# Performance work log

Measured on AMD Instinct MI355X. Metric: run time of the kernel, lower is better.

## Reference

```python
import jax, jax.numpy as jnp
import numpy as np

B, S, D = 1, 2048, 2048
H, KV, HD = 16, 4, 128
E, TOPK, F = 8, 2, 2048
THETA = 500000.0
CLIP = 8.0
EPS = 1e-5


def setup_inputs() -> dict:
    key = jax.random.key(0)
    ks = jax.random.split(key, 8)
    sc = 0.02
    return {
        "hidden_states": jax.random.normal(ks[0], (B, S, D), jnp.float32),
        "position_ids": jnp.arange(S, dtype=jnp.int64)[None, :].repeat(B, axis=0),
        "ln1_w": jnp.ones((D,), jnp.float32),
        "ln2_w": jnp.ones((D,), jnp.float32),
        "wqkv": jax.random.normal(ks[1], (D, (H + 2 * KV) * HD), jnp.float32) * sc,
        "wo": jax.random.normal(ks[2], (H * HD, D), jnp.float32) * sc,
        "router_w": jax.random.normal(ks[3], (E, D), jnp.float32) * sc,
        "w1": jax.random.normal(ks[4], (E, D, F), jnp.float32) * sc,
        "v1": jax.random.normal(ks[5], (E, D, F), jnp.float32) * sc,
        "w2": jax.random.normal(ks[6], (E, F, D), jnp.float32) * sc,
    }


def _layernorm(x, w):
    mu = jnp.mean(x, axis=-1, keepdims=True)
    var = jnp.mean((x - mu) ** 2, axis=-1, keepdims=True)
    return (x - mu) * jax.lax.rsqrt(var + EPS) * w


def _rotate_half(x):
    x1, x2 = jnp.split(x, 2, axis=-1)
    return jnp.concatenate([-x2, x1], axis=-1)


def _rope(pos):
    inv_freq = 1.0 / (THETA ** (jnp.arange(0, HD, 2, dtype=jnp.float32) / HD))
    ang = pos.astype(jnp.float32)[..., None] * inv_freq  # [B,S,HD/2]
    ang = jnp.concatenate([ang, ang], axis=-1)  # [B,S,HD]
    return jnp.cos(ang)[:, None], jnp.sin(ang)[:, None]  # [B,1,S,HD]


def _forward(hidden_states, position_ids, ln1_w, ln2_w, wqkv, wo, router_w, w1, v1, w2):
    x = hidden_states
    # --- attention sublayer ---
    h = _layernorm(x, ln1_w)
    qkv = jnp.clip(h @ wqkv, -CLIP, CLIP)  # [B,S,(H+2KV)*HD]
    q, k, v = jnp.split(qkv, [H * HD, (H + KV) * HD], axis=-1)
    q = q.reshape(B, S, H, HD).transpose(0, 2, 1, 3)   # [B,H,S,HD]
    k = k.reshape(B, S, KV, HD).transpose(0, 2, 1, 3)  # [B,KV,S,HD]
    v = v.reshape(B, S, KV, HD).transpose(0, 2, 1, 3)
    cos, sin = _rope(position_ids)
    q = q * cos + _rotate_half(q) * sin
    k = k * cos + _rotate_half(k) * sin
    rep = H // KV
    k = jnp.repeat(k, rep, axis=1)  # [B,H,S,HD]
    v = jnp.repeat(v, rep, axis=1)
    scores = jnp.einsum("bhqd,bhkd->bhqk", q, k) / np.sqrt(HD).astype(np.float32)
    causal = jnp.tril(jnp.ones((S, S), bool))
    scores = jnp.where(causal, scores, jnp.finfo(scores.dtype).min)
    probs = jax.nn.softmax(scores, axis=-1)
    attn = jnp.einsum("bhqk,bhkd->bhqd", probs, v)
    attn = attn.transpose(0, 2, 1, 3).reshape(B, S, H * HD) @ wo
    x = x + attn
    # --- MoE FFN sublayer ---
    h = _layernorm(x, ln2_w).reshape(B * S, D)  # [T,D]
    logits = h @ router_w.T                      # [T,E]
    rp = jax.nn.softmax(logits, axis=-1)
    top_w, top_i = jax.lax.top_k(rp, TOPK)       # [T,K]
    top_w = top_w / jnp.sum(top_w, axis=-1, keepdims=True)
    T = B * S
    gate = jnp.zeros((T, E), h.dtype).at[jnp.arange(T)[:, None], top_i].add(top_w)
    g = jax.nn.silu(jnp.einsum("td,edf->tef", h, w1)) * jnp.einsum("td,edf->tef", h, v1)
    y = jnp.einsum("tef,efd,te->td", g, w2, gate)
    x = x + y.reshape(B, S, D)
    return x


def reference(hidden_states, position_ids, ln1_w, ln2_w, wqkv, wo, router_w, w1, v1, w2):
    return _forward(hidden_states, position_ids, ln1_w, ln2_w, wqkv, wo, router_w, w1, v1, w2)
```

## Files before the change

### kernel.cpp

```cpp
#include <hip/hip_runtime.h>

#define S_LEN 2048
#define DMODEL 2048
#define NH 16
#define NKV 4
#define HD 128
#define NE 8
#define FF 2048
#define QKV_N 3072

typedef __attribute__((ext_vector_type(8))) short short8;
typedef __attribute__((ext_vector_type(4))) float f32x4;

__device__ inline unsigned short f2bf(float f) {
  unsigned int u = __builtin_bit_cast(unsigned int, f);
  u += 0x7fffu + ((u >> 16) & 1u);
  return (unsigned short)(u >> 16);
}
__device__ inline float bf2f(unsigned short h) {
  unsigned int u = ((unsigned int)h) << 16;
  return __builtin_bit_cast(float, u);
}
__device__ inline void split2(float v, unsigned short& h, unsigned short& l) {
  h = f2bf(v);
  l = f2bf(v - bf2f(h));
}


__device__ inline void gload16(const void* g, void* l) {
  __builtin_amdgcn_global_load_lds((const __attribute__((address_space(1))) unsigned int*)g,
                                   (__attribute__((address_space(3))) unsigned int*)l,
                                   16, 0, 0);
}
__device__ inline void stageB_chunk(const unsigned short* __restrict__ chunk,
                                    unsigned short* __restrict__ lds) {
  int w = threadIdx.x >> 6, l = threadIdx.x & 63;
  const unsigned short* s = chunk + w * 1024 + l * 8;
  unsigned short* d = lds + w * 1024;
  gload16(s, d);
  gload16(s + 512, d + 512);
}

#define WAIT_ALL  asm volatile("s_waitcnt vmcnt(0) lgkmcnt(0)" ::: "memory")
#define WAIT_LDS  asm volatile("s_waitcnt lgkmcnt(0)" ::: "memory")
#define SCHEDBAR  __builtin_amdgcn_sched_barrier(0)
#define BAR       __builtin_amdgcn_s_barrier()


__device__ inline void mma16(const unsigned short* As, const unsigned short* Bs,
                             int wr, int wc, f32x4 acc[4][4]) {
  int l = threadIdx.x & 63;
  int lr = l & 15, lg = l >> 4;
  int qoff = ((lg ^ ((lr ^ (lr >> 2)) & 3)) << 3);
  short8 a[4], b[4];
#pragma unroll
  for (int m = 0; m < 4; m++)
    a[m] = *(const short8*)(As + (wr + m * 16 + lr) * 32 + qoff);
#pragma unroll
  for (int n = 0; n < 4; n++)
    b[n] = *(const short8*)(Bs + (wc + n * 16 + lr) * 32 + qoff);
#pragma unroll
  for (int m = 0; m < 4; m++)
#pragma unroll
    for (int n = 0; n < 4; n++)
      acc[m][n] = __builtin_amdgcn_mfma_f32_16x16x32_bf16(a[m], b[n], acc[m][n], 0, 0, 0);
}

__device__ inline void mma16_dualB(const unsigned short* As, const unsigned short* Bs1,
                                   const unsigned short* Bs2, int wr, int wc,
                                   f32x4 acc1[4][4], f32x4 acc2[4][4]) {
  int l = threadIdx.x & 63;
  int lr = l & 15, lg = l >> 4;
  int qoff = ((lg ^ ((lr ^ (lr >> 2)) & 3)) << 3);
  short8 a[4], b1[4], b2[4];
#pragma unroll
  for (int m = 0; m < 4; m++)
    a[m] = *(const short8*)(As + (wr + m * 16 + lr) * 32 + qoff);
#pragma unroll
  for (int n = 0; n < 4; n++) {
    b1[n] = *(const short8*)(Bs1 + (wc + n * 16 + lr) * 32 + qoff);
    b2[n] = *(const short8*)(Bs2 + (wc + n * 16 + lr) * 32 + qoff);
  }
#pragma unroll
  for (int m = 0; m < 4; m++)
#pragma unroll
    for (int n = 0; n < 4; n++) {
      acc1[m][n] = __builtin_amdgcn_mfma_f32_16x16x32_bf16(a[m], b1[n], acc1[m][n], 0, 0, 0);
      acc2[m][n] = __builtin_amdgcn_mfma_f32_16x16x32_bf16(a[m], b2[n], acc2[m][n], 0, 0, 0);
    }
}

__device__ inline void mma16_split_reg(const unsigned short* Ash, const unsigned short* Asl,
                                       const unsigned short* Bsh, const unsigned short* Bsl,
                                       int wr, int wc, f32x4 acc[4][4]) {
  int l = threadIdx.x & 63;
  int lr = l & 15, lg = l >> 4;
  int qoff = ((lg ^ ((lr ^ (lr >> 2)) & 3)) << 3);
  short8 ah[4], al[4], bh[4], bl[4];
#pragma unroll
  for (int m = 0; m < 4; m++) {
    ah[m] = *(const short8*)(Ash + (wr + m * 16 + lr) * 32 + qoff);
    al[m] = *(const short8*)(Asl + (wr + m * 16 + lr) * 32 + qoff);
  }
#pragma unroll
  for (int n = 0; n < 4; n++) {
    bh[n] = *(const short8*)(Bsh + (wc + n * 16 + lr) * 32 + qoff);
    bl[n] = *(const short8*)(Bsl + (wc + n * 16 + lr) * 32 + qoff);
  }
#pragma unroll
  for (int m = 0; m < 4; m++)
#pragma unroll
    for (int n = 0; n < 4; n++) {
      acc[m][n] = __builtin_amdgcn_mfma_f32_16x16x32_bf16(ah[m], bh[n], acc[m][n], 0, 0, 0);
      acc[m][n] = __builtin_amdgcn_mfma_f32_16x16x32_bf16(ah[m], bl[n], acc[m][n], 0, 0, 0);
      acc[m][n] = __builtin_amdgcn_mfma_f32_16x16x32_bf16(al[m], bh[n], acc[m][n], 0, 0, 0);
    }
}


__global__ __launch_bounds__(256) void k_pack1(const float* __restrict__ src, long ld,
                                               long zs, int nc,
                                               unsigned short* __restrict__ dst) {
  __shared__ float tile[32][132];
  const float* Sp = src + (long)blockIdx.z * zs;
  int c = blockIdx.x, t = threadIdx.x;
  for (int i = 0; i < 4; i++) {
    int kt = blockIdx.y * 4 + i;
    long k0 = (long)kt * 32, n0 = (long)c * 128;
    {
      int k = t >> 3, nn = (t & 7) * 16;
      const float4* p = (const float4*)(Sp + (k0 + k) * ld + n0 + nn);
#pragma unroll
      for (int j = 0; j < 4; j++) *(float4*)&tile[k][nn + j * 4] = p[j];
    }
    __syncthreads();
    size_t cbase = ((size_t)(blockIdx.z * nc + c) * 64 + kt) * 4096;
#pragma unroll
    for (int uu = 0; uu < 2; uu++) {
      int u = t * 2 + uu;
      int n = u >> 2, qp = u & 3;
      int q = qp ^ ((n ^ (n >> 2)) & 3);
      unsigned short hb[8] __attribute__((aligned(16)));
#pragma unroll
      for (int j = 0; j < 8; j++) hb[j] = f2bf(tile[8 * q + j][n]);
      *(uint4*)(dst + cbase + u * 8) = *(const uint4*)hb;
    }
    __syncthreads();
  }
}

__global__ __launch_bounds__(256) void k_pack2(const float* __restrict__ src, long ld,
                                               long zs, int nc,
                                               unsigned short* __restrict__ dh,
                                               unsigned short* __restrict__ dl) {
  __shared__ float tile[32][132];
  const float* Sp = src + (long)blockIdx.z * zs;
  int c = blockIdx.x, t = threadIdx.x;
  for (int i = 0; i < 4; i++) {
    int kt = blockIdx.y * 4 + i;
    long k0 = (long)kt * 32, n0 = (long)c * 128;
    {
      int k = t >> 3, nn = (t & 7) * 16;
      const float4* p = (const float4*)(Sp + (k0 + k) * ld + n0 + nn);
#pragma unroll
      for (int j = 0; j < 4; j++) *(float4*)&tile[k][nn + j * 4] = p[j];
    }
    __syncthreads();
    size_t cbase = ((size_t)(blockIdx.z * nc + c) * 64 + kt) * 4096;
#pragma unroll
    for (int uu = 0; uu < 2; uu++) {
      int u = t * 2 + uu;
      int n = u >> 2, qp = u & 3;
      int q = qp ^ ((n ^ (n >> 2)) & 3);
      unsigned short hb[8] __attribute__((aligned(16)));
      unsigned short lb[8] __attribute__((aligned(16)));
#pragma unroll
      for (int j = 0; j < 8; j++) split2(tile[8 * q + j][n], hb[j], lb[j]);
      *(uint4*)(dh + cbase + u * 8) = *(const uint4*)hb;
      *(uint4*)(dl + cbase + u * 8) = *(const uint4*)lb;
    }
    __syncthreads();
  }
}

__global__ __launch_bounds__(256) void k_packbf(const unsigned short* __restrict__ src,
                                                unsigned short* __restrict__ dst) {
  int ttile = blockIdx.x;
  int z = blockIdx.y;
  const unsigned short* Sp = src + ((size_t)z * S_LEN + (size_t)ttile * 128) * HD;
  size_t ob = ((size_t)z * 64 + (size_t)ttile * 4) * 4096;
  int t = threadIdx.x;
#pragma unroll
  for (int kst = 0; kst < 4; kst++) {
#pragma unroll
    for (int uu = 0; uu < 2; uu++) {
      int u = t * 2 + uu;
      int n = u >> 2, qp = u & 3;
      int q = qp ^ ((n ^ (n >> 2)) & 3);
      *(uint4*)(dst + ob + (size_t)kst * 4096 + u * 8) =
          *(const uint4*)(Sp + (size_t)n * HD + kst * 32 + q * 8);
    }
  }
}

__global__ __launch_bounds__(256) void k_gpack(const unsigned short* __restrict__ h2b,
                                               const int* __restrict__ ptok,
                                               const int* __restrict__ meta,
                                               unsigned short* __restrict__ hAP) {
  int ty = blockIdx.x;
  if (ty >= meta[25]) return;
  int tt = meta[26 + ty];
  int e = tt & 7, m0 = tt >> 3;
  int nvalid = min(128, meta[e] - m0);
  const int* toks = ptok + meta[16 + e] + m0;
  int t = threadIdx.x;
  int r = t >> 2, q = t & 3;
  int s = (r ^ (r >> 2)) & 3;
  for (int kt = blockIdx.y * 8; kt < blockIdx.y * 8 + 8; kt++) {
    unsigned short* dst = hAP + ((size_t)ty * 64 + kt) * 4096;
#pragma unroll
    for (int rr = 0; rr < 2; rr++) {
      int row = r + rr * 64;
      uint4 v = make_uint4(0, 0, 0, 0);
      if (row < nvalid)
        v = *(const uint4*)(h2b + (size_t)toks[row] * DMODEL + kt * 32 + q * 8);
      *(uint4*)(dst + row * 32 + ((q ^ s) << 3)) = v;
    }
  }
}


__global__ __launch_bounds__(256) void k_qkv_s(const unsigned short* __restrict__ APh,
                                               const unsigned short* __restrict__ APl,
                                               const unsigned short* __restrict__ BPh,
                                               const unsigned short* __restrict__ BPl,
                                               float* __restrict__ C) {
  __shared__ unsigned short Ash[2 * 4096], Asl[2 * 4096], Bsh[2 * 4096], Bsl[2 * 4096];
  size_t ab = (size_t)blockIdx.y * 64 * 4096;
  size_t cb = (size_t)blockIdx.x * 64 * 4096;
  int w = threadIdx.x >> 6;
  int wr = (w >> 1) * 64, wc = (w & 1) * 64;
  stageB_chunk(APh + ab, Ash);
  stageB_chunk(APl + ab, Asl);
  stageB_chunk(BPh + cb, Bsh);
  stageB_chunk(BPl + cb, Bsl);
  WAIT_ALL;
  BAR;
  f32x4 acc[4][4] = {};
  for (int kt = 0; kt < 64; kt++) {
    int cur = (kt & 1) << 12, nxt = 4096 - cur;
    if (kt + 1 < 64) {
      size_t o = (size_t)(kt + 1) * 4096;
      stageB_chunk(APh + ab + o, Ash + nxt);
      stageB_chunk(APl + ab + o, Asl + nxt);
      stageB_chunk(BPh + cb + o, Bsh + nxt);
      stageB_chunk(BPl + cb + o, Bsl + nxt);
    }
    SCHEDBAR;
    mma16_split_reg(Ash + cur, Asl + cur, Bsh + cur, Bsl + cur, wr, wc, acc);
    SCHEDBAR;
    WAIT_ALL;
    BAR;
  }
  int row0 = blockIdx.y * 128, col0 = blockIdx.x * 128;
  int l = threadIdx.x & 63;
  int er = wr + ((l >> 4) << 2), ec = wc + (l & 15);
#pragma unroll
  for (int m = 0; m < 4; m++)
#pragma unroll
    for (int n = 0; n < 4; n++)
#pragma unroll
      for (int r = 0; r < 4; r++) {
        float v = acc[m][n][r];
        v = fminf(fmaxf(v, -8.f), 8.f);
        C[(size_t)(row0 + er + m * 16 + r) * QKV_N + col0 + ec + n * 16] = v;
      }
}

__global__ __launch_bounds__(256) void k_wo_s(const unsigned short* __restrict__ APh,
                                              const unsigned short* __restrict__ APl,
                                              const unsigned short* __restrict__ BPh,
                                              const unsigned short* __restrict__ BPl,
                                              const float* __restrict__ resid,
                                              float* __restrict__ x1) {
  __shared__ unsigned short Ash[2 * 4096], Asl[2 * 4096], Bsh[2 * 4096], Bsl[2 * 4096];
  size_t ab = (size_t)blockIdx.y * 64 * 4096;
  size_t cb = (size_t)blockIdx.x * 64 * 4096;
  int w = threadIdx.x >> 6;
  int wr = (w >> 1) * 64, wc = (w & 1) * 64;
  stageB_chunk(APh + ab, Ash);
  stageB_chunk(APl + ab, Asl);
  stageB_chunk(BPh + cb, Bsh);
  stageB_chunk(BPl + cb, Bsl);
  WAIT_ALL;
  BAR;
  f32x4 acc[4][4] = {};
  for (int kt = 0; kt < 64; kt++) {
    int cur = (kt & 1) << 12, nxt = 4096 - cur;
    if (kt + 1 < 64) {
      size_t o = (size_t)(kt + 1) * 4096;
      stageB_chunk(APh + ab + o, Ash + nxt);
      stageB_chunk(APl + ab + o, Asl + nxt);
      stageB_chunk(BPh + cb + o, Bsh + nxt);
      stageB_chunk(BPl + cb + o, Bsl + nxt);
    }
    SCHEDBAR;
    mma16_split_reg(Ash + cur, Asl + cur, Bsh + cur, Bsl + cur, wr, wc, acc);
    SCHEDBAR;
    WAIT_ALL;
    BAR;
  }
  int row0 = blockIdx.y * 128, col0 = blockIdx.x * 128;
  int l = threadIdx.x & 63;
  int er = wr + ((l >> 4) << 2), ec = wc + (l & 15);
#pragma unroll
  for (int m = 0; m < 4; m++)
#pragma unroll
    for (int n = 0; n < 4; n++)
#pragma unroll
      for (int r = 0; r < 4; r++) {
        size_t idx = (size_t)(row0 + er + m * 16 + r) * DMODEL + col0 + ec + n * 16;
        x1[idx] = resid[idx] + acc[m][n][r];
      }
}


__global__ __launch_bounds__(128) void k_flash(const unsigned short* __restrict__ qh,
                                               const unsigned short* __restrict__ ql,
                                               const unsigned short* __restrict__ kPh,
                                               const unsigned short* __restrict__ kPl,
                                               const unsigned short* __restrict__ vPh,
                                               const unsigned short* __restrict__ vPl,
                                               unsigned short* __restrict__ atPh,
                                               unsigned short* __restrict__ atPl) {
  int bid = blockIdx.x;
  int h = (bid & 7) | ((bid >> 8) << 3);
  int rt = (bid >> 3) & 31;
  int kv = h >> 2;
  int ntiles = (rt >> 1) + 1;
  __shared__ float Pds[2][32 * 132];
  int t = threadIdx.x;
  int w = t >> 6, l = t & 63;
  int lr = l & 15, lg = l >> 4;
  int qoff = ((lg ^ ((lr ^ (lr >> 2)) & 3)) << 3);
  int wrow0 = rt * 64 + w * 32;
  const unsigned short* Qbh = qh + (size_t)h * S_LEN * HD;
  const unsigned short* Qbl = ql + (size_t)h * S_LEN * HD;
  const unsigned short* Kch = kPh + (size_t)kv * 64 * 4096;
  const unsigned short* Kcl = kPl + (size_t)kv * 64 * 4096;
  const unsigned short* Vch = vPh + (size_t)kv * 64 * 4096;
  const unsigned short* Vcl = vPl + (size_t)kv * 64 * 4096;
  float* Pw = &Pds[w][0];
  float mrun[2][4], lrun[2][4];
  f32x4 Oc[2][8];
#pragma unroll
  for (int m = 0; m < 2; m++)
#pragma unroll
    for (int r = 0; r < 4; r++) { mrun[m][r] = -3.4e38f; lrun[m][r] = 0.f; }
#pragma unroll
  for (int m = 0; m < 2; m++)
#pragma unroll
    for (int n = 0; n < 8; n++)
#pragma unroll
      for (int r = 0; r < 4; r++) Oc[m][n][r] = 0.f;
  const float scale = 0.08838834764831845f;

  for (int kt = 0; kt < ntiles; kt++) {
    f32x4 Sa[2][8];
#pragma unroll
    for (int m = 0; m < 2; m++)
#pragma unroll
      for (int n = 0; n < 8; n++)
#pragma unroll
        for (int r = 0; r < 4; r++) Sa[m][n][r] = 0.f;
#pragma unroll
    for (int kst = 0; kst < 4; kst++) {
      short8 qfh[2], qfl[2];
#pragma unroll
      for (int m = 0; m < 2; m++) {
        size_t o = (size_t)(wrow0 + m * 16 + lr) * HD + kst * 32 + lg * 8;
        qfh[m] = *(const short8*)(Qbh + o);
        qfl[m] = *(const short8*)(Qbl + o);
      }
      const unsigned short* Kh = Kch + (size_t)(kt * 4 + kst) * 4096;
      const unsigned short* Kl = Kcl + (size_t)(kt * 4 + kst) * 4096;
      short8 bh[8], bl[8];
#pragma unroll
      for (int n = 0; n < 8; n++) {
        bh[n] = *(const short8*)(Kh + (n * 16 + lr) * 32 + qoff);
        bl[n] = *(const short8*)(Kl + (n * 16 + lr) * 32 + qoff);
      }
#pragma unroll
      for (int m = 0; m < 2; m++)
#pragma unroll
        for (int n = 0; n < 8; n++) {
          Sa[m][n] = __builtin_amdgcn_mfma_f32_16x16x32_bf16(qfh[m], bh[n], Sa[m][n], 0, 0, 0);
          Sa[m][n] = __builtin_amdgcn_mfma_f32_16x16x32_bf16(qfh[m], bl[n], Sa[m][n], 0, 0, 0);
          Sa[m][n] = __builtin_amdgcn_mfma_f32_16x16x32_bf16(qfl[m], bh[n], Sa[m][n], 0, 0, 0);
        }
    }
#pragma unroll
    for (int m = 0; m < 2; m++)
#pragma unroll
      for (int r = 0; r < 4; r++) {
        int row = wrow0 + m * 16 + lg * 4 + r;
        float mx = mrun[m][r];
#pragma unroll
        for (int n = 0; n < 8; n++) {
          float v = Sa[m][n][r] * scale;
          int col = kt * 128 + n * 16 + lr;
          v = (col <= row) ? v : -3.4e38f;
          Sa[m][n][r] = v;
          mx = fmaxf(mx, v);
        }
        mx = fmaxf(mx, __shfl_xor(mx, 1));
        mx = fmaxf(mx, __shfl_xor(mx, 2));
        mx = fmaxf(mx, __shfl_xor(mx, 4));
        mx = fmaxf(mx, __shfl_xor(mx, 8));
        float al_ = expf(mrun[m][r] - mx);
        float sum = 0.f;
#pragma unroll
        for (int n = 0; n < 8; n++) {
          float v = Sa[m][n][r];
          float e = (v > -1.0e37f) ? expf(v - mx) : 0.f;
          Sa[m][n][r] = e;
          sum += e;
        }
        sum += __shfl_xor(sum, 1);
        sum += __shfl_xor(sum, 2);
        sum += __shfl_xor(sum, 4);
        sum += __shfl_xor(sum, 8);
        lrun[m][r] = lrun[m][r] * al_ + sum;
        mrun[m][r] = mx;
#pragma unroll
        for (int n = 0; n < 8; n++) Oc[m][n][r] *= al_;
      }
    WAIT_LDS;
    SCHEDBAR;
#pragma unroll
    for (int m = 0; m < 2; m++)
#pragma unroll
      for (int n = 0; n < 8; n++)
#pragma unroll
        for (int r = 0; r < 4; r++)
          Pw[(m * 16 + lg * 4 + r) * 132 + n * 16 + lr] = Sa[m][n][r];
    WAIT_LDS;
    SCHEDBAR;
#pragma unroll
    for (int kst = 0; kst < 4; kst++) {
      const unsigned short* Vh = Vch + (size_t)(kt * 4 + kst) * 4096;
      const unsigned short* Vl = Vcl + (size_t)(kt * 4 + kst) * 4096;
      short8 bh[8], bl[8];
#pragma unroll
      for (int n = 0; n < 8; n++) {
        bh[n] = *(const short8*)(Vh + (n * 16 + lr) * 32 + qoff);
        bl[n] = *(const short8*)(Vl + (n * 16 + lr) * 32 + qoff);
      }
#pragma unroll
      for (int m = 0; m < 2; m++) {
        const float* pp = &Pw[(m * 16 + lr) * 132 + kst * 32 + lg * 8];
        unsigned short ahb[8] __attribute__((aligned(16)));
        unsigned short alb[8] __attribute__((aligned(16)));
#pragma unroll
        for (int j = 0; j < 8; j++) split2(pp[j], ahb[j], alb[j]);
        short8 ah = *(const short8*)ahb;
        short8 al_ = *(const short8*)alb;
#pragma unroll
        for (int n = 0; n < 8; n++) {
          Oc[m][n] = __builtin_amdgcn_mfma_f32_16x16x32_bf16(ah, bh[n], Oc[m][n], 0, 0, 0);
          Oc[m][n] = __builtin_amdgcn_mfma_f32_16x16x32_bf16(ah, bl[n], Oc[m][n], 0, 0, 0);
          Oc[m][n] = __builtin_amdgcn_mfma_f32_16x16x32_bf16(al_, bh[n], Oc[m][n], 0, 0, 0);
        }
      }
    }
  }
#pragma unroll
  for (int m = 0; m < 2; m++)
#pragma unroll
    for (int r = 0; r < 4; r++) {
      int row = wrow0 + m * 16 + lg * 4 + r;
      int rtc = row >> 7, rl = row & 127;
      int sr = (rl ^ (rl >> 2)) & 3;
      float lv = lrun[m][r];
#pragma unroll
      for (int n = 0; n < 8; n++) {
        int col = h * HD + n * 16 + lr;
        size_t off = ((size_t)(rtc * 64 + (col >> 5))) * 4096 + rl * 32 +
                     ((((col & 31) >> 3) ^ sr) << 3) + (col & 7);
        unsigned short hh, ll;
        split2(Oc[m][n][r] / lv, hh, ll);
        atPh[off] = hh;
        atPl[off] = ll;
      }
    }
}


__global__ __launch_bounds__(256) void k_moe1f(const unsigned short* __restrict__ hAP,
                                               const unsigned short* __restrict__ wPa,
                                               const unsigned short* __restrict__ wPb,
                                               const int* __restrict__ meta,
                                               unsigned short* __restrict__ g) {
  int ty = blockIdx.y;
  if (ty >= meta[25]) return;
  int tt = meta[26 + ty];
  int e = tt & 7, m0 = tt >> 3;
  int nvalid = min(128, meta[e] - m0);
  const unsigned short* Ab = hAP + (size_t)ty * 64 * 4096;
  const unsigned short* B1 = wPa + (size_t)(e * 16 + blockIdx.x) * 64 * 4096;
  const unsigned short* B2 = wPb + (size_t)(e * 16 + blockIdx.x) * 64 * 4096;
  __shared__ unsigned short As[2 * 4096], Bs1[2 * 4096], Bs2[2 * 4096];
  int w = threadIdx.x >> 6;
  int wr = (w >> 1) * 64, wc = (w & 1) * 64;
  stageB_chunk(Ab, As);
  stageB_chunk(B1, Bs1);
  stageB_chunk(B2, Bs2);
  WAIT_ALL;
  BAR;
  f32x4 acc1[4][4] = {}, acc2[4][4] = {};
  for (int kt = 0; kt < 64; kt++) {
    int cur = (kt & 1) << 12, nxt = 4096 - cur;
    if (kt + 1 < 64) {
      size_t o = (size_t)(kt + 1) * 4096;
      stageB_chunk(Ab + o, As + nxt);
      stageB_chunk(B1 + o, Bs1 + nxt);
      stageB_chunk(B2 + o, Bs2 + nxt);
    }
    SCHEDBAR;
    mma16_dualB(As + cur, Bs1 + cur, Bs2 + cur, wr, wc, acc1, acc2);
    SCHEDBAR;
    WAIT_ALL;
    BAR;
  }
  int l = threadIdx.x & 63;
  int er = wr + ((l >> 4) << 2), ec = wc + (l & 15);
  int ktf0 = blockIdx.x * 4;
#pragma unroll
  for (int m = 0; m < 4; m++)
#pragma unroll
    for (int n = 0; n < 4; n++)
#pragma unroll
      for (int r = 0; r < 4; r++) {
        int rl = er + m * 16 + r;
        int cc = ec + n * 16;
        float a = acc1[m][n][r];
        float s = a / (1.f + expf(-a));
        unsigned short val = (rl < nvalid) ? f2bf(s * acc2[m][n][r]) : (unsigned short)0;
        int srl = (rl ^ (rl >> 2)) & 3;
        g[((size_t)(ty * 64 + ktf0 + (cc >> 5))) * 4096 + rl * 32 +
          ((((cc & 31) >> 3) ^ srl) << 3) + (cc & 7)] = val;
      }
}

__global__ __launch_bounds__(256) void k_moe2(const unsigned short* __restrict__ gP,
                                              const unsigned short* __restrict__ wP,
                                              const int* __restrict__ ptok,
                                              const float* __restrict__ pw,
                                              const int* __restrict__ meta,
                                              float* __restrict__ out) {
  int ty = blockIdx.y;
  if (ty >= meta[25]) return;
  int tt = meta[26 + ty];
  int e = tt & 7, m0 = tt >> 3;
  int nvalid = min(128, meta[e] - m0);
  long pbase = (long)meta[16 + e] + m0;
  const unsigned short* Ab = gP + (size_t)ty * 64 * 4096;
  const unsigned short* Bb = wP + (size_t)(e * 16 + blockIdx.x) * 64 * 4096;
  __shared__ unsigned short As[2 * 4096], Bs[2 * 4096];
  int w = threadIdx.x >> 6;
  int wr = (w >> 1) * 64, wc = (w & 1) * 64;
  stageB_chunk(Ab, As);
  stageB_chunk(Bb, Bs);
  WAIT_ALL;
  BAR;
  f32x4 acc[4][4] = {};
  for (int kt = 0; kt < 64; kt++) {
    int cur = (kt & 1) << 12, nxt = 4096 - cur;
    if (kt + 1 < 64) {
      size_t o = (size_t)(kt + 1) * 4096;
      stageB_chunk(Ab + o, As + nxt);
      stageB_chunk(Bb + o, Bs + nxt);
    }
    SCHEDBAR;
    mma16(As + cur, Bs + cur, wr, wc, acc);
    SCHEDBAR;
    WAIT_ALL;
    BAR;
  }
  int col0 = blockIdx.x * 128;
  int l = threadIdx.x & 63;
  int er = wr + ((l >> 4) << 2), ec = wc + (l & 15);
#pragma unroll
  for (int m = 0; m < 4; m++)
#pragma unroll
    for (int n = 0; n < 4; n++)
#pragma unroll
      for (int r = 0; r < 4; r++) {
        int rl = er + m * 16 + r;
        if (rl < nvalid) {
          long p = pbase + rl;
          int tk = ptok[p];
          atomicAdd(&out[(size_t)tk * DMODEL + col0 + ec + n * 16], acc[m][n][r] * pw[p]);
        }
      }
}


__global__ __launch_bounds__(256) void k_ln(const float* __restrict__ x,
                                            const float* __restrict__ w,
                                            unsigned short* __restrict__ obh,
                                            unsigned short* __restrict__ obl,
                                            float* __restrict__ of, int mode) {
  int row = blockIdx.x;
  const float* xr = x + (size_t)row * DMODEL;
  float s = 0.f, ss = 0.f;
  for (int c = threadIdx.x; c < DMODEL; c += 256) {
    float v = xr[c];
    s += v; ss += v * v;
  }
#pragma unroll
  for (int o = 32; o; o >>= 1) { s += __shfl_down(s, o); ss += __shfl_down(ss, o); }
  __shared__ float rs[4], rss[4], mu_s, inv_s;
  int wid = threadIdx.x >> 6;
  if ((threadIdx.x & 63) == 0) { rs[wid] = s; rss[wid] = ss; }
  __syncthreads();
  if (threadIdx.x == 0) {
    float S1 = rs[0] + rs[1] + rs[2] + rs[3];
    float S2 = rss[0] + rss[1] + rss[2] + rss[3];
    float mu = S1 / DMODEL;
    mu_s = mu;
    inv_s = rsqrtf(S2 / DMODEL - mu * mu + 1e-5f);
  }
  __syncthreads();
  float mu = mu_s, inv = inv_s;
  int rt = row >> 7, rl = row & 127;
  int sw = (rl ^ (rl >> 2)) & 3;
  for (int c = threadIdx.x; c < DMODEL; c += 256) {
    float v = (xr[c] - mu) * inv * w[c];
    unsigned short hh, ll;
    split2(v, hh, ll);
    if (mode) {
      size_t off = ((size_t)(rt * 64 + (c >> 5))) * 4096 + rl * 32 +
                   ((((c & 31) >> 3) ^ sw) << 3) + (c & 7);
      obh[off] = hh;
      obl[off] = ll;
    } else {
      obh[(size_t)row * DMODEL + c] = hh;
      obl[(size_t)row * DMODEL + c] = ll;
      of[(size_t)row * DMODEL + c] = v;
    }
  }
}

__global__ void k_rope2(const float* __restrict__ qkv, unsigned short* __restrict__ qh,
                        unsigned short* __restrict__ ql, unsigned short* __restrict__ kh,
                        unsigned short* __restrict__ kl) {
  int t = blockIdx.x;
  int d = threadIdx.x;
  float pf = (float)pow(500000.0, (double)d * (1.0 / 64.0));
  float invf = 1.0f / pf;
  float ang = (float)t * invf;
  float cs = (float)cos((double)ang);
  float sn = (float)sin((double)ang);
  const float* row = qkv + (size_t)t * QKV_N;
  unsigned short hh, ll;
#pragma unroll
  for (int hq = 0; hq < NH; hq++) {
    float a = row[hq * HD + d], b = row[hq * HD + d + 64];
    size_t base = ((size_t)hq * S_LEN + t) * HD;
    split2(a * cs - b * sn, hh, ll); qh[base + d] = hh; ql[base + d] = ll;
    split2(b * cs + a * sn, hh, ll); qh[base + d + 64] = hh; ql[base + d + 64] = ll;
  }
#pragma unroll
  for (int kv = 0; kv < NKV; kv++) {
    float a = row[NH * HD + kv * HD + d], b = row[NH * HD + kv * HD + d + 64];
    size_t base = ((size_t)kv * S_LEN + t) * HD;
    split2(a * cs - b * sn, hh, ll); kh[base + d] = hh; kl[base + d] = ll;
    split2(b * cs + a * sn, hh, ll); kh[base + d + 64] = hh; kl[base + d + 64] = ll;
  }
}

__global__ __launch_bounds__(256) void k_router(const float* __restrict__ h2,
                                                const float* __restrict__ rw,
                                                int* __restrict__ topi,
                                                float* __restrict__ topw,
                                                int* __restrict__ cnt) {
  int t = blockIdx.x;
  __shared__ float hs[DMODEL];
  __shared__ float lg[NE];
  for (int c = threadIdx.x; c < DMODEL; c += 256) hs[c] = h2[(size_t)t * DMODEL + c];
  __syncthreads();
  int grp = threadIdx.x >> 5;
  int ln = threadIdx.x & 31;
  float p = 0.f;
  for (int c = ln; c < DMODEL; c += 32) p += hs[c] * rw[(size_t)grp * DMODEL + c];
#pragma unroll
  for (int o = 16; o; o >>= 1) p += __shfl_down(p, o, 32);
  if (ln == 0) lg[grp] = p;
  __syncthreads();
  if (threadIdx.x == 0) {
    float l0 = -3.4e38f; int i0 = 0;
    for (int e = 0; e < NE; e++)
      if (lg[e] > l0) { l0 = lg[e]; i0 = e; }
    float l1 = -3.4e38f; int i1 = 0;
    for (int e = 0; e < NE; e++)
      if (e != i0 && lg[e] > l1) { l1 = lg[e]; i1 = e; }
    float z = expf(l1 - l0);
    topi[t * 2] = i0; topi[t * 2 + 1] = i1;
    topw[t * 2] = 1.f / (1.f + z); topw[t * 2 + 1] = z / (1.f + z);
    atomicAdd(&cnt[i0], 1);
    atomicAdd(&cnt[i1], 1);
  }
}

__global__ void k_scan(int* __restrict__ meta) {
  if (threadIdx.x == 0 && blockIdx.x == 0) {
    int o = 0, nt = 0;
    for (int e = 0; e < NE; e++) {
      meta[16 + e] = o;
      for (int m0 = 0; m0 < meta[e]; m0 += 128) meta[26 + nt++] = (m0 << 3) | e;
      o += meta[e];
    }
    meta[24] = o;
    meta[25] = nt;
  }
}

__global__ void k_fill(const int* __restrict__ topi, const float* __restrict__ topw,
                       int* __restrict__ meta, int* __restrict__ ptok,
                       float* __restrict__ pw) {
  int t = blockIdx.x * blockDim.x + threadIdx.x;
  if (t >= S_LEN) return;
#pragma unroll
  for (int j = 0; j < 2; j++) {
    int e = topi[t * 2 + j];
    int p = atomicAdd(&meta[8 + e], 1);
    ptok[meta[16 + e] + p] = t;
    pw[meta[16 + e] + p] = topw[t * 2 + j];
  }
}


extern "C" void kernel_launch(void* const* d_in, const int* in_sizes, int n_in,
                              void* d_out, int out_size, void* d_ws, size_t ws_size,
                              hipStream_t stream) {
  (void)in_sizes; (void)n_in; (void)out_size; (void)ws_size;
  const float* x = (const float*)d_in[0];
  const float* ln1w = (const float*)d_in[2];
  const float* ln2w = (const float*)d_in[3];
  const float* wqkv = (const float*)d_in[4];
  const float* wo = (const float*)d_in[5];
  const float* rw = (const float*)d_in[6];
  const float* w1 = (const float*)d_in[7];
  const float* v1 = (const float*)d_in[8];
  const float* w2 = (const float*)d_in[9];
  float* out = (float*)d_out;

  char* wsb = (char*)d_ws;
  const size_t MiB = 1u << 20;
  unsigned short* h1Ph = (unsigned short*)(wsb + 0 * MiB);
  unsigned short* h1Pl = (unsigned short*)(wsb + 8 * MiB);
  float* qkvb = (float*)(wsb + 16 * MiB);
  unsigned short* qh = (unsigned short*)(wsb + 40 * MiB);
  unsigned short* ql = (unsigned short*)(wsb + 48 * MiB);
  unsigned short* kh = (unsigned short*)(wsb + 56 * MiB);
  unsigned short* kl = (unsigned short*)(wsb + 58 * MiB);
  unsigned short* vPh = (unsigned short*)(wsb + 60 * MiB);
  unsigned short* vPl = (unsigned short*)(wsb + 62 * MiB);
  unsigned short* kPh = (unsigned short*)(wsb + 64 * MiB);
  unsigned short* kPl = (unsigned short*)(wsb + 66 * MiB);
  unsigned short* atPh = (unsigned short*)(wsb + 68 * MiB);
  unsigned short* atPl = (unsigned short*)(wsb + 76 * MiB);
  unsigned short* wqkvPh = (unsigned short*)(wsb + 84 * MiB);
  unsigned short* wqkvPl = (unsigned short*)(wsb + 96 * MiB);
  unsigned short* woPh = (unsigned short*)(wsb + 108 * MiB);
  unsigned short* woPl = (unsigned short*)(wsb + 116 * MiB);
  unsigned short* hAP = (unsigned short*)(wsb + 0 * MiB);
  unsigned short* g = (unsigned short*)(wsb + 20 * MiB);
  float* h2f = (float*)(wsb + 40 * MiB);
  unsigned short* h2b = (unsigned short*)(wsb + 56 * MiB);
  unsigned short* h2lo = (unsigned short*)(wsb + 20 * MiB);
  unsigned short* wPa = (unsigned short*)(wsb + 40 * MiB);
  unsigned short* wPb = (unsigned short*)(wsb + 104 * MiB);
  char* small = wsb + 168 * MiB;
  int* topi = (int*)small;
  float* topw = (float*)(small + 16384);
  int* ptok = (int*)(small + 32768);
  float* pw = (float*)(small + 49152);
  int* meta = (int*)(small + 65536);

  k_pack2<<<dim3(QKV_N / 128, 16, 1), 256, 0, stream>>>(wqkv, QKV_N, 0, QKV_N / 128,
                                                        wqkvPh, wqkvPl);
  k_pack2<<<dim3(DMODEL / 128, 16, 1), 256, 0, stream>>>(wo, DMODEL, 0, DMODEL / 128,
                                                         woPh, woPl);

  k_ln<<<S_LEN, 256, 0, stream>>>(x, ln1w, h1Ph, h1Pl, (float*)nullptr, 1);
  k_qkv_s<<<dim3(QKV_N / 128, S_LEN / 128), 256, 0, stream>>>(h1Ph, h1Pl, wqkvPh, wqkvPl,
                                                              qkvb);
  k_rope2<<<S_LEN, 64, 0, stream>>>(qkvb, qh, ql, kh, kl);
  k_pack2<<<dim3(1, 16, NKV), 256, 0, stream>>>(qkvb + (NH + NKV) * HD, QKV_N, HD, 1,
                                                vPh, vPl);
  k_packbf<<<dim3(16, NKV), 256, 0, stream>>>(kh, kPh);
  k_packbf<<<dim3(16, NKV), 256, 0, stream>>>(kl, kPl);
  k_flash<<<512, 128, 0, stream>>>(qh, ql, kPh, kPl, vPh, vPl, atPh, atPl);
  k_wo_s<<<dim3(16, 16), 256, 0, stream>>>(atPh, atPl, woPh, woPl, x, out);

  k_ln<<<S_LEN, 256, 0, stream>>>(out, ln2w, h2b, h2lo, h2f, 0);
  hipMemsetAsync(meta, 0, 512, stream);
  k_router<<<S_LEN, 256, 0, stream>>>(h2f, rw, topi, topw, meta);
  k_scan<<<1, 64, 0, stream>>>(meta);
  k_fill<<<8, 256, 0, stream>>>(topi, topw, meta, ptok, pw);
  k_gpack<<<dim3(40, 8), 256, 0, stream>>>(h2b, ptok, meta, hAP);
  k_pack1<<<dim3(16, 16, NE), 256, 0, stream>>>(w1, FF, (long)DMODEL * FF, 16, wPa);
  k_pack1<<<dim3(16, 16, NE), 256, 0, stream>>>(v1, FF, (long)DMODEL * FF, 16, wPb);
  k_moe1f<<<dim3(16, 40), 256, 0, stream>>>(hAP, wPa, wPb, meta, g);
  k_pack1<<<dim3(16, 16, NE), 256, 0, stream>>>(w2, DMODEL, (long)FF * DMODEL, 16, wPa);
  k_moe2<<<dim3(16, 40), 256, 0, stream>>>(g, wPa, ptok, pw, meta, out);
}
```

Before: 939.5 us.

## Prefetch two k-tiles ahead in GEMM loops using partial vmcnt waits

Restructures the double-buffered GEMM main loops (QKV, Wo, MoE up and down projections) so loads for tile kt+2 are issued into the buffer just consumed, after a barrier. Partial s_waitcnt vmcnt(N) waits for only the older tile instead of draining every outstanding load. This keeps one tile of global-to-LDS loads in flight across each compute step, hiding more memory latency. The cost is an extra barrier per iteration, and correctness depends on the vmcnt counts matching the number of loads issued per stage.

```diff
diff --git a/kernel.cpp b/kernel.cpp
--- a/kernel.cpp
+++ b/kernel.cpp
@@ -41,6 +41,10 @@
   gload16(s + 512, d + 512);
 }
 
+#define WVM0  asm volatile("s_waitcnt vmcnt(0)" ::: "memory")
+#define WVM4  asm volatile("s_waitcnt vmcnt(4)" ::: "memory")
+#define WVM6  asm volatile("s_waitcnt vmcnt(6)" ::: "memory")
+#define WVM8  asm volatile("s_waitcnt vmcnt(8)" ::: "memory")
 #define WAIT_ALL  asm volatile("s_waitcnt vmcnt(0) lgkmcnt(0)" ::: "memory")
 #define WAIT_LDS  asm volatile("s_waitcnt lgkmcnt(0)" ::: "memory")
 #define SCHEDBAR  __builtin_amdgcn_sched_barrier(0)
@@ -244,22 +248,29 @@
   stageB_chunk(APl + ab, Asl);
   stageB_chunk(BPh + cb, Bsh);
   stageB_chunk(BPl + cb, Bsl);
-  WAIT_ALL;
+  stageB_chunk(APh + ab + 4096, Ash + 4096);
+  stageB_chunk(APl + ab + 4096, Asl + 4096);
+  stageB_chunk(BPh + cb + 4096, Bsh + 4096);
+  stageB_chunk(BPl + cb + 4096, Bsl + 4096);
+  WVM8;
   BAR;
   f32x4 acc[4][4] = {};
   for (int kt = 0; kt < 64; kt++) {
-    int cur = (kt & 1) << 12, nxt = 4096 - cur;
-    if (kt + 1 < 64) {
-      size_t o = (size_t)(kt + 1) * 4096;
-      stageB_chunk(APh + ab + o, Ash + nxt);
-      stageB_chunk(APl + ab + o, Asl + nxt);
-      stageB_chunk(BPh + cb + o, Bsh + nxt);
-      stageB_chunk(BPl + cb + o, Bsl + nxt);
-    }
+    int cur = (kt & 1) << 12;
     SCHEDBAR;
     mma16_split_reg(Ash + cur, Asl + cur, Bsh + cur, Bsl + cur, wr, wc, acc);
     SCHEDBAR;
-    WAIT_ALL;
+    BAR;
+    if (kt + 2 < 64) {
+      size_t o = (size_t)(kt + 2) * 4096;
+      stageB_chunk(APh + ab + o, Ash + cur);
+      stageB_chunk(APl + ab + o, Asl + cur);
+      stageB_chunk(BPh + cb + o, Bsh + cur);
+      stageB_chunk(BPl + cb + o, Bsl + cur);
+      WVM8;
+    } else {
+      WVM0;
+    }
     BAR;
   }
   int row0 = blockIdx.y * 128, col0 = blockIdx.x * 128;
@@ -292,22 +303,29 @@
   stageB_chunk(APl + ab, Asl);
   stageB_chunk(BPh + cb, Bsh);
   stageB_chunk(BPl + cb, Bsl);
-  WAIT_ALL;
+  stageB_chunk(APh + ab + 4096, Ash + 4096);
+  stageB_chunk(APl + ab + 4096, Asl + 4096);
+  stageB_chunk(BPh + cb + 4096, Bsh + 4096);
+  stageB_chunk(BPl + cb + 4096, Bsl + 4096);
+  WVM8;
   BAR;
   f32x4 acc[4][4] = {};
   for (int kt = 0; kt < 64; kt++) {
-    int cur = (kt & 1) << 12, nxt = 4096 - cur;
-    if (kt + 1 < 64) {
-      size_t o = (size_t)(kt + 1) * 4096;
-      stageB_chunk(APh + ab + o, Ash + nxt);
-      stageB_chunk(APl + ab + o, Asl + nxt);
-      stageB_chunk(BPh + cb + o, Bsh + nxt);
-      stageB_chunk(BPl + cb + o, Bsl + nxt);
-    }
+    int cur = (kt & 1) << 12;
     SCHEDBAR;
     mma16_split_reg(Ash + cur, Asl + cur, Bsh + cur, Bsl + cur, wr, wc, acc);
     SCHEDBAR;
-    WAIT_ALL;
+    BAR;
+    if (kt + 2 < 64) {
+      size_t o = (size_t)(kt + 2) * 4096;
+      stageB_chunk(APh + ab + o, Ash + cur);
+      stageB_chunk(APl + ab + o, Asl + cur);
+      stageB_chunk(BPh + cb + o, Bsh + cur);
+      stageB_chunk(BPl + cb + o, Bsl + cur);
+      WVM8;
+    } else {
+      WVM0;
+    }
     BAR;
   }
   int row0 = blockIdx.y * 128, col0 = blockIdx.x * 128;
@@ -515,21 +533,27 @@
   stageB_chunk(Ab, As);
   stageB_chunk(B1, Bs1);
   stageB_chunk(B2, Bs2);
-  WAIT_ALL;
+  stageB_chunk(Ab + 4096, As + 4096);
+  stageB_chunk(B1 + 4096, Bs1 + 4096);
+  stageB_chunk(B2 + 4096, Bs2 + 4096);
+  WVM6;
   BAR;
   f32x4 acc1[4][4] = {}, acc2[4][4] = {};
   for (int kt = 0; kt < 64; kt++) {
-    int cur = (kt & 1) << 12, nxt = 4096 - cur;
-    if (kt + 1 < 64) {
-      size_t o = (size_t)(kt + 1) * 4096;
-      stageB_chunk(Ab + o, As + nxt);
-      stageB_chunk(B1 + o, Bs1 + nxt);
-      stageB_chunk(B2 + o, Bs2 + nxt);
-    }
+    int cur = (kt & 1) << 12;
     SCHEDBAR;
     mma16_dualB(As + cur, Bs1 + cur, Bs2 + cur, wr, wc, acc1, acc2);
     SCHEDBAR;
-    WAIT_ALL;
+    BAR;
+    if (kt + 2 < 64) {
+      size_t o = (size_t)(kt + 2) * 4096;
+      stageB_chunk(Ab + o, As + cur);
+      stageB_chunk(B1 + o, Bs1 + cur);
+      stageB_chunk(B2 + o, Bs2 + cur);
+      WVM6;
+    } else {
+      WVM0;
+    }
     BAR;
   }
   int l = threadIdx.x & 63;
@@ -571,20 +595,25 @@
   int wr = (w >> 1) * 64, wc = (w & 1) * 64;
   stageB_chunk(Ab, As);
   stageB_chunk(Bb, Bs);
-  WAIT_ALL;
+  stageB_chunk(Ab + 4096, As + 4096);
+  stageB_chunk(Bb + 4096, Bs + 4096);
+  WVM4;
   BAR;
   f32x4 acc[4][4] = {};
   for (int kt = 0; kt < 64; kt++) {
-    int cur = (kt & 1) << 12, nxt = 4096 - cur;
-    if (kt + 1 < 64) {
-      size_t o = (size_t)(kt + 1) * 4096;
-      stageB_chunk(Ab + o, As + nxt);
-      stageB_chunk(Bb + o, Bs + nxt);
-    }
+    int cur = (kt & 1) << 12;
     SCHEDBAR;
     mma16(As + cur, Bs + cur, wr, wc, acc);
     SCHEDBAR;
-    WAIT_ALL;
+    BAR;
+    if (kt + 2 < 64) {
+      size_t o = (size_t)(kt + 2) * 4096;
+      stageB_chunk(Ab + o, As + cur);
+      stageB_chunk(Bb + o, Bs + cur);
+      WVM4;
+    } else {
+      WVM0;
+    }
     BAR;
   }
   int col0 = blockIdx.x * 128;
```

Result: slower. 1.001 ms (+6.6%).

## Triple-buffer MoE GEMM LDS staging and split-K the down projection

Applied to the files above, without the earlier changes.

Both MoE GEMM kernels move from a double-buffered LDS pipeline to a three-stage ring buffer. Loads are issued two tiles ahead, with partial vmcnt waits in place of a full drain every iteration. The down-projection kernel also splits K into two halves over a new grid z dimension. This doubles its block count and relies on the existing atomicAdd epilogue to combine the partial sums. The cost is more LDS per block, which may lower occupancy, plus twice as many atomic adds to the output.

```diff
diff --git a/kernel.cpp b/kernel.cpp
--- a/kernel.cpp
+++ b/kernel.cpp
@@ -41,6 +41,11 @@
   gload16(s + 512, d + 512);
 }
 
+#define WVM0   asm volatile("s_waitcnt vmcnt(0)" ::: "memory")
+#define WVM4   asm volatile("s_waitcnt vmcnt(4)" ::: "memory")
+#define WVM6   asm volatile("s_waitcnt vmcnt(6)" ::: "memory")
+#define WVM8   asm volatile("s_waitcnt vmcnt(8)" ::: "memory")
+#define WVM12  asm volatile("s_waitcnt vmcnt(12)" ::: "memory")
 #define WAIT_ALL  asm volatile("s_waitcnt vmcnt(0) lgkmcnt(0)" ::: "memory")
 #define WAIT_LDS  asm volatile("s_waitcnt lgkmcnt(0)" ::: "memory")
 #define SCHEDBAR  __builtin_amdgcn_sched_barrier(0)
@@ -509,28 +514,38 @@
   const unsigned short* Ab = hAP + (size_t)ty * 64 * 4096;
   const unsigned short* B1 = wPa + (size_t)(e * 16 + blockIdx.x) * 64 * 4096;
   const unsigned short* B2 = wPb + (size_t)(e * 16 + blockIdx.x) * 64 * 4096;
-  __shared__ unsigned short As[2 * 4096], Bs1[2 * 4096], Bs2[2 * 4096];
+  __shared__ unsigned short L[3][3][4096];
   int w = threadIdx.x >> 6;
   int wr = (w >> 1) * 64, wc = (w & 1) * 64;
-  stageB_chunk(Ab, As);
-  stageB_chunk(B1, Bs1);
-  stageB_chunk(B2, Bs2);
-  WAIT_ALL;
+#pragma unroll
+  for (int p = 0; p < 3; p++) {
+    size_t o = (size_t)p * 4096;
+    stageB_chunk(Ab + o, &L[p][0][0]);
+    stageB_chunk(B1 + o, &L[p][1][0]);
+    stageB_chunk(B2 + o, &L[p][2][0]);
+  }
+  WVM12;
   BAR;
   f32x4 acc1[4][4] = {}, acc2[4][4] = {};
+  int cur = 0;
   for (int kt = 0; kt < 64; kt++) {
-    int cur = (kt & 1) << 12, nxt = 4096 - cur;
-    if (kt + 1 < 64) {
-      size_t o = (size_t)(kt + 1) * 4096;
-      stageB_chunk(Ab + o, As + nxt);
-      stageB_chunk(B1 + o, Bs1 + nxt);
-      stageB_chunk(B2 + o, Bs2 + nxt);
-    }
-    SCHEDBAR;
-    mma16_dualB(As + cur, Bs1 + cur, Bs2 + cur, wr, wc, acc1, acc2);
-    SCHEDBAR;
-    WAIT_ALL;
+    SCHEDBAR;
+    mma16_dualB(&L[cur][0][0], &L[cur][1][0], &L[cur][2][0], wr, wc, acc1, acc2);
+    SCHEDBAR;
     BAR;
+    if (kt + 3 < 64) {
+      size_t o = (size_t)(kt + 3) * 4096;
+      stageB_chunk(Ab + o, &L[cur][0][0]);
+      stageB_chunk(B1 + o, &L[cur][1][0]);
+      stageB_chunk(B2 + o, &L[cur][2][0]);
+      WVM12;
+    } else if (kt + 3 == 64) {
+      WVM6;
+    } else {
+      WVM0;
+    }
+    BAR;
+    cur = (cur == 2) ? 0 : cur + 1;
   }
   int l = threadIdx.x & 63;
   int er = wr + ((l >> 4) << 2), ec = wc + (l & 15);
@@ -564,28 +579,39 @@
   int e = tt & 7, m0 = tt >> 3;
   int nvalid = min(128, meta[e] - m0);
   long pbase = (long)meta[16 + e] + m0;
-  const unsigned short* Ab = gP + (size_t)ty * 64 * 4096;
-  const unsigned short* Bb = wP + (size_t)(e * 16 + blockIdx.x) * 64 * 4096;
-  __shared__ unsigned short As[2 * 4096], Bs[2 * 4096];
+  int kc = blockIdx.z;
+  const unsigned short* Ab = gP + ((size_t)ty * 64 + kc * 32) * 4096;
+  const unsigned short* Bb = wP + ((size_t)(e * 16 + blockIdx.x) * 64 + kc * 32) * 4096;
+  __shared__ unsigned short L[3][2][4096];
   int w = threadIdx.x >> 6;
   int wr = (w >> 1) * 64, wc = (w & 1) * 64;
-  stageB_chunk(Ab, As);
-  stageB_chunk(Bb, Bs);
-  WAIT_ALL;
+#pragma unroll
+  for (int p = 0; p < 3; p++) {
+    size_t o = (size_t)p * 4096;
+    stageB_chunk(Ab + o, &L[p][0][0]);
+    stageB_chunk(Bb + o, &L[p][1][0]);
+  }
+  WVM8;
   BAR;
   f32x4 acc[4][4] = {};
-  for (int kt = 0; kt < 64; kt++) {
-    int cur = (kt & 1) << 12, nxt = 4096 - cur;
-    if (kt + 1 < 64) {
-      size_t o = (size_t)(kt + 1) * 4096;
-      stageB_chunk(Ab + o, As + nxt);
-      stageB_chunk(Bb + o, Bs + nxt);
-    }
-    SCHEDBAR;
-    mma16(As + cur, Bs + cur, wr, wc, acc);
-    SCHEDBAR;
-    WAIT_ALL;
+  int cur = 0;
+  for (int kt = 0; kt < 32; kt++) {
+    SCHEDBAR;
+    mma16(&L[cur][0][0], &L[cur][1][0], wr, wc, acc);
+    SCHEDBAR;
     BAR;
+    if (kt + 3 < 32) {
+      size_t o = (size_t)(kt + 3) * 4096;
+      stageB_chunk(Ab + o, &L[cur][0][0]);
+      stageB_chunk(Bb + o, &L[cur][1][0]);
+      WVM8;
+    } else if (kt + 3 == 32) {
+      WVM4;
+    } else {
+      WVM0;
+    }
+    BAR;
+    cur = (cur == 2) ? 0 : cur + 1;
   }
   int col0 = blockIdx.x * 128;
   int l = threadIdx.x & 63;
@@ -815,5 +841,5 @@
   k_pack1<<<dim3(16, 16, NE), 256, 0, stream>>>(v1, FF, (long)DMODEL * FF, 16, wPb);
   k_moe1f<<<dim3(16, 40), 256, 0, stream>>>(hAP, wPa, wPb, meta, g);
   k_pack1<<<dim3(16, 16, NE), 256, 0, stream>>>(w2, DMODEL, (long)FF * DMODEL, 16, wPa);
-  k_moe2<<<dim3(16, 40), 256, 0, stream>>>(g, wPa, ptok, pw, meta, out);
-}
+  k_moe2<<<dim3(16, 40, 2), 256, 0, stream>>>(g, wPa, ptok, pw, meta, out);
+}
```

Result: faster. 917.6 us (-2.3%).
